# Optimization experiments

Hardware: AMD Instinct MI355X
Metric: run time of the kernel (lower is better)

Reference implementation:

```python
import jax, jax.numpy as jnp
import numpy as np

DT = 1.0
EPS = 1e-6


def setup_inputs() -> dict:
    key = jax.random.key(0)
    ks = jax.random.split(key, 5)
    B, I, H = 8192, 512, 1024
    scale = (6.0 / ((1 + 5.0) * (I + H))) ** 0.5  # kaiming_uniform with a=sqrt(5) bound
    return {
        "x": jax.random.normal(ks[0], (B, I), dtype=jnp.float32),
        "hidden": jax.random.normal(ks[1], (B, H), dtype=jnp.float32),
        "W_tau": jax.random.uniform(ks[2], (H, I + H), dtype=jnp.float32, minval=-scale, maxval=scale),
        "b_tau": jnp.zeros((H,), dtype=jnp.float32),
        "W_r": jax.random.uniform(ks[3], (H, I + H), dtype=jnp.float32, minval=-scale, maxval=scale),
        "b_r": jnp.zeros((H,), dtype=jnp.float32),
        "W_h": jax.random.uniform(ks[4], (H, I + H), dtype=jnp.float32, minval=-scale, maxval=scale),
        "b_h": jnp.zeros((H,), dtype=jnp.float32),
    }


def reference(x, hidden, W_tau, b_tau, W_r, b_r, W_h, b_h):
    combined = jnp.concatenate([x, hidden], axis=1)          # [B, I+H]
    tau = jax.nn.softplus(combined @ W_tau.T + b_tau) + EPS  # [B, H]
    r = jax.nn.sigmoid(combined @ W_r.T + b_r)               # [B, H]
    gated = r * hidden
    cand_in = jnp.concatenate([x, gated], axis=1)            # [B, I+H]
    h_tilde = jnp.tanh(cand_in @ W_h.T + b_h)                # [B, H]
    return hidden + DT * (h_tilde - hidden) / tau
```

## Files before the change

### kernel.cpp

```cpp
#include <hip/hip_runtime.h>
#include <hip/hip_bf16.h>

typedef __attribute__((ext_vector_type(8))) unsigned short u16x8;
typedef __attribute__((ext_vector_type(8))) __bf16        bf16x8;
typedef __attribute__((ext_vector_type(4))) float         f32x4;

static constexpr int B_ = 8192;
static constexpr int I_ = 512;
static constexpr int H_ = 1024;
static constexpr int K_ = 1536;
static constexpr int NT    = K_ / 64;
static constexpr int NITER = NT / 2;

#define AS1 __attribute__((address_space(1)))
#define AS3 __attribute__((address_space(3)))

__device__ __forceinline__ unsigned short f2bf(float f) {
    unsigned int u = __float_as_uint(f);
    u += 0x7FFF + ((u >> 16) & 1);
    return (unsigned short)(u >> 16);
}

__device__ __forceinline__ void memfence() { asm volatile("" ::: "memory"); }
__device__ __forceinline__ void barrier_() {
    memfence(); __builtin_amdgcn_s_barrier(); memfence();
}
__device__ __forceinline__ void vwait4() {
    asm volatile("s_waitcnt vmcnt(4)" ::: "memory");
    __builtin_amdgcn_sched_barrier(0);
}

__device__ __forceinline__ u16x8 cvt8(const float4* s) {
    float4 a = s[0], b = s[1];
    u16x8 o;
    o[0] = f2bf(a.x); o[1] = f2bf(a.y); o[2] = f2bf(a.z); o[3] = f2bf(a.w);
    o[4] = f2bf(b.x); o[5] = f2bf(b.y); o[6] = f2bf(b.z); o[7] = f2bf(b.w);
    return o;
}

__global__ void pack_xh(const float* __restrict__ x, const float* __restrict__ hid,
                        unsigned short* __restrict__ cmb1) {
    constexpr int NX8 = B_ * I_ / 8;
    constexpr int NH8 = B_ * H_ / 8;
    int i = blockIdx.x * blockDim.x + threadIdx.x;
    if (i < NX8) {
        int row = i >> 6, c8 = i & 63;
        u16x8 o = cvt8((const float4*)x + (size_t)i * 2);
        *(u16x8*)(cmb1 + (size_t)row * K_ + c8 * 8) = o;
    } else if (i < NX8 + NH8) {
        int j = i - NX8;
        int row = j >> 7, c8 = j & 127;
        u16x8 o = cvt8((const float4*)hid + (size_t)j * 2);
        *(u16x8*)(cmb1 + (size_t)row * K_ + 512 + c8 * 8) = o;
    }
}

__global__ void cvt_w3(const float* __restrict__ wt, const float* __restrict__ wr,
                       const float* __restrict__ wh,
                       unsigned short* __restrict__ wtb,
                       unsigned short* __restrict__ wrb,
                       unsigned short* __restrict__ whb) {
    constexpr int NW8 = H_ * K_ / 8;
    int i = blockIdx.x * blockDim.x + threadIdx.x;
    const float* src; unsigned short* dst; int k;
    if (i < NW8)           { src = wt; dst = wtb; k = i; }
    else if (i < 2 * NW8)  { src = wr; dst = wrb; k = i - NW8; }
    else if (i < 3 * NW8)  { src = wh; dst = whb; k = i - 2 * NW8; }
    else return;
    u16x8 o = cvt8((const float4*)src + (size_t)k * 2);
    *(u16x8*)(dst + (size_t)k * 8) = o;
}

template<int MODE>
__global__ __launch_bounds__(512, 1)
void gemm4(const unsigned short* __restrict__ A1,
           const unsigned short* __restrict__ A2,
           const unsigned short* __restrict__ W0,
           const unsigned short* __restrict__ W1,
           const float* __restrict__ bias0,
           const float* __restrict__ bias1,
           const float* __restrict__ hidden,
           const unsigned short* __restrict__ itau_in,
           float* __restrict__ outF,
           unsigned short* __restrict__ itau_out,
           unsigned short* __restrict__ gate_out)
{
    extern __shared__ __align__(16) char lds[];

    const int t = threadIdx.x;
    const int w = t >> 6, l = t & 63;
    const int bz = (MODE == 0) ? blockIdx.z : 0;
    const unsigned short* Wsel = (MODE == 0 && bz) ? W1 : W0;
    const float* bias = (MODE == 0 && bz) ? bias1 : bias0;

    const int wg  = blockIdx.y * 8 + blockIdx.x;
    const int swz = (wg & 7) * 32 + (wg >> 3);
    const int m0  = (swz >> 3) * 256;
    const int n0  = (swz & 7) * 128;

    const int srow  = t >> 3;
    const int sslot = ((t & 7) ^ (srow & 7)) * 8;
    const unsigned short* srcA1 = A1 + (size_t)(m0 + srow) * K_ + sslot;
    const unsigned short* srcA2 = A2 + (size_t)(m0 + srow) * K_ + sslot;
    const unsigned short* srcB  = Wsel + (size_t)(n0 + srow) * K_ + sslot;
    char* dstA = lds + w * 1024;
    char* dstB = lds + 65536 + w * 1024;

    auto stageA = [&](int tt, int h) {
        const unsigned short* base = (MODE == 1 && tt >= 8) ? srcA2 : srcA1;
        const unsigned short* s = base + (size_t)(h * 128) * K_ + tt * 64;
        char* d = dstA + (tt & 1) * 32768 + h * 16384;
        #pragma unroll
        for (int j = 0; j < 2; ++j)
            __builtin_amdgcn_global_load_lds(
                (const AS1 void*)(s + (size_t)j * 64 * K_),
                (AS3 void*)(d + j * 8192), 16, 0, 0);
    };
    auto stageB = [&](int tt, int h) {
        const unsigned short* s = srcB + (size_t)(h * 64) * K_ + tt * 64;
        char* d = dstB + (tt & 1) * 16384 + h * 8192;
        __builtin_amdgcn_global_load_lds((const AS1 void*)s, (AS3 void*)d, 16, 0, 0);
    };

    const int fr = l & 15, kq = l >> 4;
    const int wm = w >> 1, wn = w & 1;
    const int fx = (kq ^ (fr & 7)) << 4;
    const char* rdA0 = lds + (wm * 32 + fr) * 128 + fx;
    const char* rdA1 = lds + (wm * 32 + fr) * 128 + (fx ^ 64);
    const char* rdB0 = lds + 65536 + (wn * 32 + fr) * 128 + fx;
    const char* rdB1 = lds + 65536 + (wn * 32 + fr) * 128 + (fx ^ 64);

    bf16x8 af[2][2], bfr[2][2][2];
    f32x4 acc[4][4];
    #pragma unroll
    for (int i = 0; i < 4; ++i)
        #pragma unroll
        for (int jn = 0; jn < 4; ++jn) acc[i][jn] = (f32x4)0.0f;

    auto readA = [&](int half, int par) {
        #pragma unroll
        for (int mi = 0; mi < 2; ++mi) {
            af[mi][0] = *(const bf16x8*)(rdA0 + par * 32768 + half * 16384 + mi * 2048);
            af[mi][1] = *(const bf16x8*)(rdA1 + par * 32768 + half * 16384 + mi * 2048);
        }
    };
    auto readBall = [&](int par) {
        #pragma unroll
        for (int bh = 0; bh < 2; ++bh)
            #pragma unroll
            for (int ni = 0; ni < 2; ++ni) {
                bfr[bh][ni][0] = *(const bf16x8*)(rdB0 + par * 16384 + bh * 8192 + ni * 2048);
                bfr[bh][ni][1] = *(const bf16x8*)(rdB1 + par * 16384 + bh * 8192 + ni * 2048);
            }
    };
    auto quad16 = [&](int ah) {
        __builtin_amdgcn_s_setprio(1);
        #pragma unroll
        for (int bh = 0; bh < 2; ++bh)
            #pragma unroll
            for (int mi = 0; mi < 2; ++mi)
                #pragma unroll
                for (int ni = 0; ni < 2; ++ni)
                    #pragma unroll
                    for (int ks = 0; ks < 2; ++ks)
                        acc[ah * 2 + mi][bh * 2 + ni] =
                            __builtin_amdgcn_mfma_f32_16x16x32_bf16(
                                af[mi][ks], bfr[bh][ni][ks],
                                acc[ah * 2 + mi][bh * 2 + ni], 0, 0, 0);
        __builtin_amdgcn_s_setprio(0);
    };

    stageA(0, 0); stageA(0, 1); stageB(0, 0); stageB(0, 1);
    stageA(1, 0); stageB(1, 0); stageB(1, 1);
    vwait4(); barrier_();

    for (int j = 0; j < NITER; ++j) {
        const int tE = (2 * j + 2 < NT) ? 2 * j + 2 : 0;
        const int tO = (2 * j + 3 < NT) ? 2 * j + 3 : 0;
        readA(0, 0); readBall(0); stageA(2 * j + 1, 1);
        quad16(0); barrier_();
        readA(1, 0); stageA(tE, 0); stageB(tE, 0); stageB(tE, 1);
        quad16(1); vwait4(); barrier_();
        readA(0, 1); readBall(1); stageA(tE, 1);
        quad16(0); barrier_();
        readA(1, 1); stageA(tO, 0); stageB(tO, 0); stageB(tO, 1);
        quad16(1); vwait4(); barrier_();
    }
    asm volatile("s_waitcnt vmcnt(0)" ::: "memory");

    const int rs4 = kq * 4;
    const int nB0 = n0 + wn * 32;
    const int mB0 = m0 + wm * 32;
    #pragma unroll
    for (int ah = 0; ah < 2; ++ah)
        #pragma unroll
        for (int mi = 0; mi < 2; ++mi)
            #pragma unroll
            for (int bh = 0; bh < 2; ++bh)
                #pragma unroll
                for (int ni = 0; ni < 2; ++ni) {
                    const int n = nB0 + bh * 64 + ni * 16 + fr;
                    const float bv = bias[n];
                    #pragma unroll
                    for (int jj = 0; jj < 4; ++jj) {
                        const int m = mB0 + ah * 128 + mi * 16 + rs4 + jj;
                        const size_t ix = (size_t)m * H_ + n;
                        const float z = acc[ah * 2 + mi][bh * 2 + ni][jj] + bv;
                        if (MODE == 0) {
                            if (bz == 0) {
                                const float sp = (z > 15.f) ? z
                                               : __logf(1.0f + __expf(z));
                                itau_out[ix] = f2bf(__fdividef(1.0f, sp + 1e-6f));
                            } else {
                                const float r = __fdividef(1.0f, 1.0f + __expf(-z));
                                gate_out[(size_t)m * K_ + 512 + n] = f2bf(r * hidden[ix]);
                            }
                        } else {
                            const float e2 = __expf(2.0f * z);
                            const float th = __fdividef(e2 - 1.0f, e2 + 1.0f);
                            const float h = hidden[ix];
                            const float it = __uint_as_float(((unsigned)itau_in[ix]) << 16);
                            outF[ix] = h + (th - h) * it;
                        }
                    }
                }
}

extern "C" void kernel_launch(void* const* d_in, const int* in_sizes, int n_in,
                              void* d_out, int out_size, void* d_ws, size_t ws_size,
                              hipStream_t stream) {
    (void)in_sizes; (void)n_in; (void)out_size; (void)ws_size;

    const float* x     = (const float*)d_in[0];
    const float* hid   = (const float*)d_in[1];
    const float* W_tau = (const float*)d_in[2];
    const float* b_tau = (const float*)d_in[3];
    const float* W_r   = (const float*)d_in[4];
    const float* b_r   = (const float*)d_in[5];
    const float* W_h   = (const float*)d_in[6];
    const float* b_h   = (const float*)d_in[7];

    unsigned short* cmb1 = (unsigned short*)d_ws;
    unsigned short* cmb2 = cmb1 + (size_t)B_ * K_;
    unsigned short* wtb  = cmb2 + (size_t)B_ * K_;
    unsigned short* wrb  = wtb  + (size_t)H_ * K_;
    unsigned short* whb  = wrb  + (size_t)H_ * K_;
    unsigned short* itau = whb  + (size_t)H_ * K_;

    hipFuncSetAttribute(reinterpret_cast<const void*>(&gemm4<0>),
                        hipFuncAttributeMaxDynamicSharedMemorySize, 98304);
    hipFuncSetAttribute(reinterpret_cast<const void*>(&gemm4<1>),
                        hipFuncAttributeMaxDynamicSharedMemorySize, 98304);

    const int th = 256;
    constexpr int NPACK = B_ * I_ / 8 + B_ * H_ / 8;
    pack_xh<<<NPACK / th, th, 0, stream>>>(x, hid, cmb1);
    constexpr int NW3 = 3 * H_ * K_ / 8;
    cvt_w3<<<NW3 / th, th, 0, stream>>>(W_tau, W_r, W_h, wtb, wrb, whb);

    dim3 g0(8, 32, 2);
    gemm4<0><<<g0, 512, 98304, stream>>>(cmb1, cmb1, wtb, wrb, b_tau, b_r,
                                         hid, nullptr, nullptr, itau, cmb2);
    dim3 g1(8, 32, 1);
    gemm4<1><<<g1, 512, 98304, stream>>>(cmb1, cmb2, whb, nullptr, b_h, nullptr,
                                         hid, itau, (float*)d_out, nullptr, nullptr);
}
```

Measured before the change: 125.0 us.

## Fuse tau and reset GEMMs sharing A tiles; merge conversion kernels

The tau and reset-gate GEMMs, which previously ran as separate blocks over blockIdx.z and each loaded the combined input, now run in one kernel. Each A tile is staged into LDS once and used against both weight matrices, with two accumulator sets per wave. The input-pack and weight-convert kernels are also merged into one launch. The cost is 128KB of LDS, double the accumulator registers, and half as many blocks for the first GEMM, which may hurt latency hiding.

```diff
diff --git a/kernel.cpp b/kernel.cpp
--- a/kernel.cpp
+++ b/kernel.cpp
@@ -25,6 +25,10 @@
 __device__ __forceinline__ void barrier_() {
     memfence(); __builtin_amdgcn_s_barrier(); memfence();
 }
+__device__ __forceinline__ void vwait6() {
+    asm volatile("s_waitcnt vmcnt(6)" ::: "memory");
+    __builtin_amdgcn_sched_barrier(0);
+}
 __device__ __forceinline__ void vwait4() {
     asm volatile("s_waitcnt vmcnt(4)" ::: "memory");
     __builtin_amdgcn_sched_barrier(0);
@@ -38,10 +42,16 @@
     return o;
 }
 
-__global__ void pack_xh(const float* __restrict__ x, const float* __restrict__ hid,
-                        unsigned short* __restrict__ cmb1) {
+__global__ void prep(const float* __restrict__ x, const float* __restrict__ hid,
+                     const float* __restrict__ wt, const float* __restrict__ wr,
+                     const float* __restrict__ wh,
+                     unsigned short* __restrict__ cmb1,
+                     unsigned short* __restrict__ wtb,
+                     unsigned short* __restrict__ wrb,
+                     unsigned short* __restrict__ whb) {
     constexpr int NX8 = B_ * I_ / 8;
     constexpr int NH8 = B_ * H_ / 8;
+    constexpr int NW8 = H_ * K_ / 8;
     int i = blockIdx.x * blockDim.x + threadIdx.x;
     if (i < NX8) {
         int row = i >> 6, c8 = i & 63;
@@ -52,47 +62,31 @@
         int row = j >> 7, c8 = j & 127;
         u16x8 o = cvt8((const float4*)hid + (size_t)j * 2);
         *(u16x8*)(cmb1 + (size_t)row * K_ + 512 + c8 * 8) = o;
+    } else {
+        int k = i - (NX8 + NH8);
+        const float* src; unsigned short* dst;
+        if (k < NW8)          { src = wt; dst = wtb; }
+        else if (k < 2 * NW8) { src = wr; dst = wrb; k -= NW8; }
+        else                  { src = wh; dst = whb; k -= 2 * NW8; }
+        u16x8 o = cvt8((const float4*)src + (size_t)k * 2);
+        *(u16x8*)(dst + (size_t)k * 8) = o;
     }
 }
 
-__global__ void cvt_w3(const float* __restrict__ wt, const float* __restrict__ wr,
-                       const float* __restrict__ wh,
-                       unsigned short* __restrict__ wtb,
-                       unsigned short* __restrict__ wrb,
-                       unsigned short* __restrict__ whb) {
-    constexpr int NW8 = H_ * K_ / 8;
-    int i = blockIdx.x * blockDim.x + threadIdx.x;
-    const float* src; unsigned short* dst; int k;
-    if (i < NW8)           { src = wt; dst = wtb; k = i; }
-    else if (i < 2 * NW8)  { src = wr; dst = wrb; k = i - NW8; }
-    else if (i < 3 * NW8)  { src = wh; dst = whb; k = i - 2 * NW8; }
-    else return;
-    u16x8 o = cvt8((const float4*)src + (size_t)k * 2);
-    *(u16x8*)(dst + (size_t)k * 8) = o;
-}
-
-template<int MODE>
 __global__ __launch_bounds__(512, 1)
-void gemm4(const unsigned short* __restrict__ A1,
-           const unsigned short* __restrict__ A2,
-           const unsigned short* __restrict__ W0,
-           const unsigned short* __restrict__ W1,
-           const float* __restrict__ bias0,
-           const float* __restrict__ bias1,
-           const float* __restrict__ hidden,
-           const unsigned short* __restrict__ itau_in,
-           float* __restrict__ outF,
-           unsigned short* __restrict__ itau_out,
-           unsigned short* __restrict__ gate_out)
+void gemm_tr(const unsigned short* __restrict__ A,
+             const unsigned short* __restrict__ W0,
+             const unsigned short* __restrict__ W1,
+             const float* __restrict__ b0,
+             const float* __restrict__ b1,
+             const float* __restrict__ hidden,
+             unsigned short* __restrict__ itau_out,
+             unsigned short* __restrict__ gate_out)
 {
     extern __shared__ __align__(16) char lds[];
 
     const int t = threadIdx.x;
     const int w = t >> 6, l = t & 63;
-    const int bz = (MODE == 0) ? blockIdx.z : 0;
-    const unsigned short* Wsel = (MODE == 0 && bz) ? W1 : W0;
-    const float* bias = (MODE == 0 && bz) ? bias1 : bias0;
-
     const int wg  = blockIdx.y * 8 + blockIdx.x;
     const int swz = (wg & 7) * 32 + (wg >> 3);
     const int m0  = (swz >> 3) * 256;
@@ -100,14 +94,157 @@
 
     const int srow  = t >> 3;
     const int sslot = ((t & 7) ^ (srow & 7)) * 8;
+    const unsigned short* srcA  = A  + (size_t)(m0 + srow) * K_ + sslot;
+    const unsigned short* srcB0 = W0 + (size_t)(n0 + srow) * K_ + sslot;
+    const unsigned short* srcB1 = W1 + (size_t)(n0 + srow) * K_ + sslot;
+    char* dstA = lds + w * 1024;
+    char* dstB = lds + 65536 + w * 1024;
+
+    auto stageA = [&](int tt) {
+        const unsigned short* s = srcA + tt * 64;
+        char* d = dstA + (tt & 1) * 32768;
+        #pragma unroll
+        for (int q = 0; q < 4; ++q)
+            __builtin_amdgcn_global_load_lds(
+                (const AS1 void*)(s + (size_t)q * 64 * K_),
+                (AS3 void*)(d + q * 8192), 16, 0, 0);
+    };
+    auto stageB = [&](int tt, int wi) {
+        const unsigned short* s = (wi ? srcB1 : srcB0) + tt * 64;
+        char* d = dstB + (tt & 1) * 32768 + wi * 16384;
+        #pragma unroll
+        for (int h = 0; h < 2; ++h)
+            __builtin_amdgcn_global_load_lds(
+                (const AS1 void*)(s + (size_t)(h * 64) * K_),
+                (AS3 void*)(d + h * 8192), 16, 0, 0);
+    };
+
+    const int fr = l & 15, kq = l >> 4;
+    const int wm = w >> 1, wn = w & 1;
+    const int fx = (kq ^ (fr & 7)) << 4;
+    const char* rdA0 = lds + (wm * 32 + fr) * 128 + fx;
+    const char* rdA1 = lds + (wm * 32 + fr) * 128 + (fx ^ 64);
+    const char* rdB0 = lds + 65536 + (wn * 32 + fr) * 128 + fx;
+    const char* rdB1 = lds + 65536 + (wn * 32 + fr) * 128 + (fx ^ 64);
+
+    bf16x8 af[4][2], bfr[2][2][2];
+    f32x4 acc[2][4][4];
+    #pragma unroll
+    for (int wi = 0; wi < 2; ++wi)
+        #pragma unroll
+        for (int i = 0; i < 4; ++i)
+            #pragma unroll
+            for (int jn = 0; jn < 4; ++jn) acc[wi][i][jn] = (f32x4)0.0f;
+
+    auto readAfull = [&](int par) {
+        #pragma unroll
+        for (int mf = 0; mf < 4; ++mf) {
+            const int off = par * 32768 + (mf >> 1) * 16384 + (mf & 1) * 2048;
+            af[mf][0] = *(const bf16x8*)(rdA0 + off);
+            af[mf][1] = *(const bf16x8*)(rdA1 + off);
+        }
+    };
+    auto readB = [&](int wi, int par) {
+        #pragma unroll
+        for (int bh = 0; bh < 2; ++bh)
+            #pragma unroll
+            for (int ni = 0; ni < 2; ++ni) {
+                const int off = par * 32768 + wi * 16384 + bh * 8192 + ni * 2048;
+                bfr[bh][ni][0] = *(const bf16x8*)(rdB0 + off);
+                bfr[bh][ni][1] = *(const bf16x8*)(rdB1 + off);
+            }
+    };
+    auto mfma32 = [&](int wi) {
+        __builtin_amdgcn_s_setprio(1);
+        #pragma unroll
+        for (int mf = 0; mf < 4; ++mf)
+            #pragma unroll
+            for (int bh = 0; bh < 2; ++bh)
+                #pragma unroll
+                for (int ni = 0; ni < 2; ++ni)
+                    #pragma unroll
+                    for (int ks = 0; ks < 2; ++ks)
+                        acc[wi][mf][bh * 2 + ni] =
+                            __builtin_amdgcn_mfma_f32_16x16x32_bf16(
+                                af[mf][ks], bfr[bh][ni][ks],
+                                acc[wi][mf][bh * 2 + ni], 0, 0, 0);
+        __builtin_amdgcn_s_setprio(0);
+    };
+
+    stageA(0); stageB(0, 0); stageB(0, 1);
+    stageA(1); stageB(1, 0);
+    vwait6(); barrier_();
+
+    for (int j = 0; j < NITER; ++j) {
+        const int tE = (2 * j + 2 < NT) ? 2 * j + 2 : 0;
+        const int tO = (2 * j + 3 < NT) ? 2 * j + 3 : 0;
+        readAfull(0); readB(0, 0); stageB(2 * j + 1, 1);
+        mfma32(0); barrier_();
+        readB(1, 0); stageA(tE); stageB(tE, 0);
+        mfma32(1); vwait6(); barrier_();
+        readAfull(1); readB(0, 1); stageB(tE, 1);
+        mfma32(0); barrier_();
+        readB(1, 1); stageA(tO); stageB(tO, 0);
+        mfma32(1); vwait6(); barrier_();
+    }
+    asm volatile("s_waitcnt vmcnt(0)" ::: "memory");
+
+    const int rs4 = kq * 4;
+    const int nB0 = n0 + wn * 32;
+    #pragma unroll
+    for (int wi = 0; wi < 2; ++wi)
+        #pragma unroll
+        for (int mf = 0; mf < 4; ++mf)
+            #pragma unroll
+            for (int bh = 0; bh < 2; ++bh)
+                #pragma unroll
+                for (int ni = 0; ni < 2; ++ni) {
+                    const int n = nB0 + bh * 64 + ni * 16 + fr;
+                    const float bv = (wi ? b1 : b0)[n];
+                    #pragma unroll
+                    for (int jj = 0; jj < 4; ++jj) {
+                        const int m = m0 + (mf >> 1) * 128 + wm * 32 + (mf & 1) * 16 + rs4 + jj;
+                        const size_t ix = (size_t)m * H_ + n;
+                        const float z = acc[wi][mf][bh * 2 + ni][jj] + bv;
+                        if (wi == 0) {
+                            const float sp = (z > 15.f) ? z : __logf(1.0f + __expf(z));
+                            itau_out[ix] = f2bf(__fdividef(1.0f, sp + 1e-6f));
+                        } else {
+                            const float r = __fdividef(1.0f, 1.0f + __expf(-z));
+                            gate_out[(size_t)m * K_ + 512 + n] = f2bf(r * hidden[ix]);
+                        }
+                    }
+                }
+}
+
+__global__ __launch_bounds__(512, 1)
+void gemm_h(const unsigned short* __restrict__ A1,
+            const unsigned short* __restrict__ A2,
+            const unsigned short* __restrict__ W0,
+            const float* __restrict__ bias0,
+            const float* __restrict__ hidden,
+            const unsigned short* __restrict__ itau_in,
+            float* __restrict__ outF)
+{
+    extern __shared__ __align__(16) char lds[];
+
+    const int t = threadIdx.x;
+    const int w = t >> 6, l = t & 63;
+    const int wg  = blockIdx.y * 8 + blockIdx.x;
+    const int swz = (wg & 7) * 32 + (wg >> 3);
+    const int m0  = (swz >> 3) * 256;
+    const int n0  = (swz & 7) * 128;
+
+    const int srow  = t >> 3;
+    const int sslot = ((t & 7) ^ (srow & 7)) * 8;
     const unsigned short* srcA1 = A1 + (size_t)(m0 + srow) * K_ + sslot;
     const unsigned short* srcA2 = A2 + (size_t)(m0 + srow) * K_ + sslot;
-    const unsigned short* srcB  = Wsel + (size_t)(n0 + srow) * K_ + sslot;
+    const unsigned short* srcB  = W0 + (size_t)(n0 + srow) * K_ + sslot;
     char* dstA = lds + w * 1024;
     char* dstB = lds + 65536 + w * 1024;
 
     auto stageA = [&](int tt, int h) {
-        const unsigned short* base = (MODE == 1 && tt >= 8) ? srcA2 : srcA1;
+        const unsigned short* base = (tt >= 8) ? srcA2 : srcA1;
         const unsigned short* s = base + (size_t)(h * 128) * K_ + tt * 64;
         char* d = dstA + (tt & 1) * 32768 + h * 16384;
         #pragma unroll
@@ -200,28 +337,17 @@
                 #pragma unroll
                 for (int ni = 0; ni < 2; ++ni) {
                     const int n = nB0 + bh * 64 + ni * 16 + fr;
-                    const float bv = bias[n];
+                    const float bv = bias0[n];
                     #pragma unroll
                     for (int jj = 0; jj < 4; ++jj) {
                         const int m = mB0 + ah * 128 + mi * 16 + rs4 + jj;
                         const size_t ix = (size_t)m * H_ + n;
                         const float z = acc[ah * 2 + mi][bh * 2 + ni][jj] + bv;
-                        if (MODE == 0) {
-                            if (bz == 0) {
-                                const float sp = (z > 15.f) ? z
-                                               : __logf(1.0f + __expf(z));
-                                itau_out[ix] = f2bf(__fdividef(1.0f, sp + 1e-6f));
-                            } else {
-                                const float r = __fdividef(1.0f, 1.0f + __expf(-z));
-                                gate_out[(size_t)m * K_ + 512 + n] = f2bf(r * hidden[ix]);
-                            }
-                        } else {
-                            const float e2 = __expf(2.0f * z);
-                            const float th = __fdividef(e2 - 1.0f, e2 + 1.0f);
-                            const float h = hidden[ix];
-                            const float it = __uint_as_float(((unsigned)itau_in[ix]) << 16);
-                            outF[ix] = h + (th - h) * it;
-                        }
+                        const float e2 = __expf(2.0f * z);
+                        const float th = __fdividef(e2 - 1.0f, e2 + 1.0f);
+                        const float h = hidden[ix];
+                        const float it = __uint_as_float(((unsigned)itau_in[ix]) << 16);
+                        outF[ix] = h + (th - h) * it;
                     }
                 }
 }
@@ -247,21 +373,19 @@
     unsigned short* whb  = wrb  + (size_t)H_ * K_;
     unsigned short* itau = whb  + (size_t)H_ * K_;
 
-    hipFuncSetAttribute(reinterpret_cast<const void*>(&gemm4<0>),
+    hipFuncSetAttribute(reinterpret_cast<const void*>(&gemm_tr),
+                        hipFuncAttributeMaxDynamicSharedMemorySize, 131072);
+    hipFuncSetAttribute(reinterpret_cast<const void*>(&gemm_h),
                         hipFuncAttributeMaxDynamicSharedMemorySize, 98304);
-    hipFuncSetAttribute(reinterpret_cast<const void*>(&gemm4<1>),
-                        hipFuncAttributeMaxDynamicSharedMemorySize, 98304);
 
     const int th = 256;
-    constexpr int NPACK = B_ * I_ / 8 + B_ * H_ / 8;
-    pack_xh<<<NPACK / th, th, 0, stream>>>(x, hid, cmb1);
-    constexpr int NW3 = 3 * H_ * K_ / 8;
-    cvt_w3<<<NW3 / th, th, 0, stream>>>(W_tau, W_r, W_h, wtb, wrb, whb);
-
-    dim3 g0(8, 32, 2);
-    gemm4<0><<<g0, 512, 98304, stream>>>(cmb1, cmb1, wtb, wrb, b_tau, b_r,
-                                         hid, nullptr, nullptr, itau, cmb2);
-    dim3 g1(8, 32, 1);
-    gemm4<1><<<g1, 512, 98304, stream>>>(cmb1, cmb2, whb, nullptr, b_h, nullptr,
-                                         hid, itau, (float*)d_out, nullptr, nullptr);
-}
+    constexpr int NPREP = B_ * I_ / 8 + B_ * H_ / 8 + 3 * H_ * K_ / 8;
+    prep<<<NPREP / th, th, 0, stream>>>(x, hid, W_tau, W_r, W_h,
+                                        cmb1, wtb, wrb, whb);
+
+    dim3 g(8, 32);
+    gemm_tr<<<g, 512, 131072, stream>>>(cmb1, wtb, wrb, b_tau, b_r, hid,
+                                        itau, cmb2);
+    gemm_h<<<g, 512, 98304, stream>>>(cmb1, cmb2, whb, b_h, hid, itau,
+                                      (float*)d_out);
+}
```

After: 105.9 us. 1.18x faster.

## Merge prep kernels, split tau/r GEMMs into separate launches, read hidden as bf16

Applied to the files above, without the earlier changes.

Merges the activation pack and weight conversion into one prep kernel, which saves a launch. Replaces the single z=2 grid for the tau and r GEMMs with two separate launches. The epilogues now read hidden from the bf16 combined buffer instead of the fp32 input, which halves that read traffic but adds bf16 rounding error on hidden in the gate and final output. Running the two GEMMs back to back serializes work that the z=2 grid ran concurrently (512 workgroups), which may lower occupancy or overlap.

```diff
diff --git a/kernel.cpp b/kernel.cpp
--- a/kernel.cpp
+++ b/kernel.cpp
@@ -20,6 +20,9 @@
     u += 0x7FFF + ((u >> 16) & 1);
     return (unsigned short)(u >> 16);
 }
+__device__ __forceinline__ float bf2f(unsigned short u) {
+    return __uint_as_float(((unsigned int)u) << 16);
+}
 
 __device__ __forceinline__ void memfence() { asm volatile("" ::: "memory"); }
 __device__ __forceinline__ void barrier_() {
@@ -38,10 +41,16 @@
     return o;
 }
 
-__global__ void pack_xh(const float* __restrict__ x, const float* __restrict__ hid,
-                        unsigned short* __restrict__ cmb1) {
+__global__ void prep(const float* __restrict__ x, const float* __restrict__ hid,
+                     const float* __restrict__ wt, const float* __restrict__ wr,
+                     const float* __restrict__ wh,
+                     unsigned short* __restrict__ cmb1,
+                     unsigned short* __restrict__ wtb,
+                     unsigned short* __restrict__ wrb,
+                     unsigned short* __restrict__ whb) {
     constexpr int NX8 = B_ * I_ / 8;
     constexpr int NH8 = B_ * H_ / 8;
+    constexpr int NW8 = H_ * K_ / 8;
     int i = blockIdx.x * blockDim.x + threadIdx.x;
     if (i < NX8) {
         int row = i >> 6, c8 = i & 63;
@@ -52,23 +61,15 @@
         int row = j >> 7, c8 = j & 127;
         u16x8 o = cvt8((const float4*)hid + (size_t)j * 2);
         *(u16x8*)(cmb1 + (size_t)row * K_ + 512 + c8 * 8) = o;
+    } else {
+        int k = i - (NX8 + NH8);
+        const float* src; unsigned short* dst;
+        if (k < NW8)          { src = wt; dst = wtb; }
+        else if (k < 2 * NW8) { src = wr; dst = wrb; k -= NW8; }
+        else                  { src = wh; dst = whb; k -= 2 * NW8; }
+        u16x8 o = cvt8((const float4*)src + (size_t)k * 2);
+        *(u16x8*)(dst + (size_t)k * 8) = o;
     }
-}
-
-__global__ void cvt_w3(const float* __restrict__ wt, const float* __restrict__ wr,
-                       const float* __restrict__ wh,
-                       unsigned short* __restrict__ wtb,
-                       unsigned short* __restrict__ wrb,
-                       unsigned short* __restrict__ whb) {
-    constexpr int NW8 = H_ * K_ / 8;
-    int i = blockIdx.x * blockDim.x + threadIdx.x;
-    const float* src; unsigned short* dst; int k;
-    if (i < NW8)           { src = wt; dst = wtb; k = i; }
-    else if (i < 2 * NW8)  { src = wr; dst = wrb; k = i - NW8; }
-    else if (i < 3 * NW8)  { src = wh; dst = whb; k = i - 2 * NW8; }
-    else return;
-    u16x8 o = cvt8((const float4*)src + (size_t)k * 2);
-    *(u16x8*)(dst + (size_t)k * 8) = o;
 }
 
 template<int MODE>
@@ -76,10 +77,7 @@
 void gemm4(const unsigned short* __restrict__ A1,
            const unsigned short* __restrict__ A2,
            const unsigned short* __restrict__ W0,
-           const unsigned short* __restrict__ W1,
            const float* __restrict__ bias0,
-           const float* __restrict__ bias1,
-           const float* __restrict__ hidden,
            const unsigned short* __restrict__ itau_in,
            float* __restrict__ outF,
            unsigned short* __restrict__ itau_out,
@@ -89,10 +87,6 @@
 
     const int t = threadIdx.x;
     const int w = t >> 6, l = t & 63;
-    const int bz = (MODE == 0) ? blockIdx.z : 0;
-    const unsigned short* Wsel = (MODE == 0 && bz) ? W1 : W0;
-    const float* bias = (MODE == 0 && bz) ? bias1 : bias0;
-
     const int wg  = blockIdx.y * 8 + blockIdx.x;
     const int swz = (wg & 7) * 32 + (wg >> 3);
     const int m0  = (swz >> 3) * 256;
@@ -102,12 +96,12 @@
     const int sslot = ((t & 7) ^ (srow & 7)) * 8;
     const unsigned short* srcA1 = A1 + (size_t)(m0 + srow) * K_ + sslot;
     const unsigned short* srcA2 = A2 + (size_t)(m0 + srow) * K_ + sslot;
-    const unsigned short* srcB  = Wsel + (size_t)(n0 + srow) * K_ + sslot;
+    const unsigned short* srcB  = W0 + (size_t)(n0 + srow) * K_ + sslot;
     char* dstA = lds + w * 1024;
     char* dstB = lds + 65536 + w * 1024;
 
     auto stageA = [&](int tt, int h) {
-        const unsigned short* base = (MODE == 1 && tt >= 8) ? srcA2 : srcA1;
+        const unsigned short* base = (MODE == 2 && tt >= 8) ? srcA2 : srcA1;
         const unsigned short* s = base + (size_t)(h * 128) * K_ + tt * 64;
         char* d = dstA + (tt & 1) * 32768 + h * 16384;
         #pragma unroll
@@ -200,26 +194,24 @@
                 #pragma unroll
                 for (int ni = 0; ni < 2; ++ni) {
                     const int n = nB0 + bh * 64 + ni * 16 + fr;
-                    const float bv = bias[n];
+                    const float bv = bias0[n];
                     #pragma unroll
                     for (int jj = 0; jj < 4; ++jj) {
                         const int m = mB0 + ah * 128 + mi * 16 + rs4 + jj;
                         const size_t ix = (size_t)m * H_ + n;
+                        const size_t hx = (size_t)m * K_ + 512 + n;
                         const float z = acc[ah * 2 + mi][bh * 2 + ni][jj] + bv;
                         if (MODE == 0) {
-                            if (bz == 0) {
-                                const float sp = (z > 15.f) ? z
-                                               : __logf(1.0f + __expf(z));
-                                itau_out[ix] = f2bf(__fdividef(1.0f, sp + 1e-6f));
-                            } else {
-                                const float r = __fdividef(1.0f, 1.0f + __expf(-z));
-                                gate_out[(size_t)m * K_ + 512 + n] = f2bf(r * hidden[ix]);
-                            }
+                            const float sp = (z > 15.f) ? z : __logf(1.0f + __expf(z));
+                            itau_out[ix] = f2bf(__fdividef(1.0f, sp + 1e-6f));
+                        } else if (MODE == 1) {
+                            const float r = __fdividef(1.0f, 1.0f + __expf(-z));
+                            gate_out[hx] = f2bf(r * bf2f(A1[hx]));
                         } else {
                             const float e2 = __expf(2.0f * z);
                             const float th = __fdividef(e2 - 1.0f, e2 + 1.0f);
-                            const float h = hidden[ix];
-                            const float it = __uint_as_float(((unsigned)itau_in[ix]) << 16);
+                            const float h = bf2f(A1[hx]);
+                            const float it = bf2f(itau_in[ix]);
                             outF[ix] = h + (th - h) * it;
                         }
                     }
@@ -251,17 +243,19 @@
                         hipFuncAttributeMaxDynamicSharedMemorySize, 98304);
     hipFuncSetAttribute(reinterpret_cast<const void*>(&gemm4<1>),
                         hipFuncAttributeMaxDynamicSharedMemorySize, 98304);
+    hipFuncSetAttribute(reinterpret_cast<const void*>(&gemm4<2>),
+                        hipFuncAttributeMaxDynamicSharedMemorySize, 98304);
 
     const int th = 256;
-    constexpr int NPACK = B_ * I_ / 8 + B_ * H_ / 8;
-    pack_xh<<<NPACK / th, th, 0, stream>>>(x, hid, cmb1);
-    constexpr int NW3 = 3 * H_ * K_ / 8;
-    cvt_w3<<<NW3 / th, th, 0, stream>>>(W_tau, W_r, W_h, wtb, wrb, whb);
-
-    dim3 g0(8, 32, 2);
-    gemm4<0><<<g0, 512, 98304, stream>>>(cmb1, cmb1, wtb, wrb, b_tau, b_r,
-                                         hid, nullptr, nullptr, itau, cmb2);
-    dim3 g1(8, 32, 1);
-    gemm4<1><<<g1, 512, 98304, stream>>>(cmb1, cmb2, whb, nullptr, b_h, nullptr,
-                                         hid, itau, (float*)d_out, nullptr, nullptr);
-}
+    constexpr int NPREP = B_ * I_ / 8 + B_ * H_ / 8 + 3 * H_ * K_ / 8;
+    prep<<<NPREP / th, th, 0, stream>>>(x, hid, W_tau, W_r, W_h,
+                                        cmb1, wtb, wrb, whb);
+
+    dim3 g(8, 32);
+    gemm4<0><<<g, 512, 98304, stream>>>(cmb1, cmb1, wtb, b_tau, nullptr,
+                                        nullptr, itau, nullptr);
+    gemm4<1><<<g, 512, 98304, stream>>>(cmb1, cmb1, wrb, b_r, nullptr,
+                                        nullptr, nullptr, cmb2);
+    gemm4<2><<<g, 512, 98304, stream>>>(cmb1, cmb2, whb, b_h, itau,
+                                        (float*)d_out, nullptr, nullptr);
+}
```

Measured after the change: 109.8 us. -12.2%, faster.
